# Kernel tuning notes

Measured on AMD Instinct MI355X. Metric: run time of the kernel, lower is better.

The kernel has to match this reference:

```python
import jax, jax.numpy as jnp
import numpy as np

EMBED, HIDDEN, VOCAB = 512, 512, 30000
B, S, K, NT = 16, 128, 49, 5


def _lin(x, W, b):
    # torch nn.Linear: y = x @ W.T + b, W stored as (out, in)
    return x @ W.T + b


def setup_inputs() -> dict:
    key = jax.random.key(0)
    ks = jax.random.split(key, 32)
    g = lambda i, shape, scale=0.05: (jax.random.normal(ks[i], shape, dtype=jnp.float32) * scale)
    inp = {
        "epoch": 30,
        "h_t": jax.random.normal(ks[0], (B, S, HIDDEN), dtype=jnp.float32),
        "V": jax.random.normal(ks[1], (B, K, HIDDEN), dtype=jnp.float32),
        "T": jax.random.normal(ks[2], (B, NT, EMBED), dtype=jnp.float32),
        "W_ZV": g(3, (49, HIDDEN)), "b_ZV": jnp.zeros((49,), jnp.float32),
        "W_Zh": g(4, (49, HIDDEN)), "b_Zh": jnp.zeros((49,), jnp.float32),
        "W_az": g(5, (1, 49)), "b_az": jnp.zeros((1,), jnp.float32),
        "W_QT": g(6, (5, EMBED)), "b_QT": jnp.zeros((5,), jnp.float32),
        "W_Qh": g(7, (5, HIDDEN)), "b_Qh": jnp.zeros((5,), jnp.float32),
        "W_bq": g(8, (1, 5)), "b_bq": jnp.zeros((1,), jnp.float32),
        "W_sq": g(9, (EMBED, EMBED)), "b_sq": jnp.zeros((EMBED,), jnp.float32),
        "W_sh": g(10, (EMBED, HIDDEN)), "b_sh": jnp.zeros((EMBED,), jnp.float32),
        "W_Ss": g(11, (5, EMBED)), "b_Ss": jnp.zeros((5,), jnp.float32),
        "W_Sr": g(12, (5, EMBED)), "b_Sr": jnp.zeros((5,), jnp.float32),
        "W_sz": g(13, (EMBED, HIDDEN)), "b_sz": jnp.zeros((EMBED,), jnp.float32),
        "W_mlp": g(14, (VOCAB, EMBED)), "b_mlp": jnp.zeros((VOCAB,), jnp.float32),
    }
    return inp


def reference(epoch, h_t, V, T,
              W_ZV, b_ZV, W_Zh, b_Zh, W_az, b_az,
              W_QT, b_QT, W_Qh, b_Qh, W_bq, b_bq,
              W_sq, b_sq, W_sh, b_sh, W_Ss, b_Ss,
              W_Sr, b_Sr, W_sz, b_sz, W_mlp, b_mlp):
    # --- visual attention (dropout = identity, eval mode) ---
    # content_V: [B, S, K, 49]
    content_V = _lin(V, W_ZV, b_ZV)[:, None, :, :] + _lin(h_t, W_Zh, b_Zh)[:, :, None, :]
    visual_t = (jnp.tanh(content_V) @ W_az.T + b_az)[..., 0]          # [B, S, K]
    alpha_t = jax.nn.softmax(visual_t, axis=-1)
    z_t = jnp.einsum('bsk,bkh->bsh', alpha_t, V)                      # [B, S, H]
    r_t = jnp.tanh(_lin(z_t, W_sz, b_sz))                             # [B, S, E]
    # --- topic attention ---
    content_T = _lin(T, W_QT, b_QT)[:, None, :, :] + _lin(h_t, W_Qh, b_Qh)[:, :, None, :]  # [B,S,5,5]
    topic_t = (jnp.tanh(content_T) @ W_bq.T + b_bq)[..., 0]           # [B, S, 5]
    beta_t = jax.nn.softmax(topic_t, axis=-1)
    q_t = jnp.einsum('bst,bte->bse', beta_t, T)                       # [B, S, E]
    s_t = jnp.tanh(_lin(q_t, W_sq, b_sq) + _lin(h_t, W_sh, b_sh))     # [B, S, E]
    # --- sentinel scores: the torch loop reduces to (batch 0, diagonal pos) only ---
    qh0 = _lin(h_t[0], W_Qh, b_Qh)                                    # [S, 5]
    score_s = jnp.tanh(_lin(s_t[0], W_Ss, b_Ss) + qh0) @ W_bq.T + b_bq  # [S, 1]
    score_r = jnp.tanh(_lin(r_t[0], W_Sr, b_Sr) + qh0) @ W_bq.T + b_bq  # [S, 1]
    if epoch <= 20:
        gama_t = 1.0
    else:
        gama_t = jax.nn.sigmoid(score_s - score_r)[None, :, :]        # [1, S, 1]
    c_t = gama_t * s_t + (1.0 - gama_t) * r_t                         # [B, S, E]
    scores = _lin(c_t, W_mlp, b_mlp)                                  # [B, S, vocab]
    return scores
```

## Files before the change

kernel.cpp:

```cpp
#include <hip/hip_runtime.h>
#include <hip/hip_bf16.h>


typedef short bf16x8 __attribute__((ext_vector_type(8)));
typedef float f32x4 __attribute__((ext_vector_type(4)));
typedef short short8 __attribute__((ext_vector_type(8)));

static __device__ __forceinline__ short f2bf(float f) {
    union { float f; unsigned u; } v; v.f = f;
    unsigned r = v.u + 0x7FFFu + ((v.u >> 16) & 1u);
    return (short)(r >> 16);
}

#define GLD_LDS16(gp, lp)                                                          \
    __builtin_amdgcn_global_load_lds(                                              \
        (const __attribute__((address_space(1))) unsigned int*)(gp),               \
        (__attribute__((address_space(3))) unsigned int*)(lp), 16, 0, 0)

__global__ __launch_bounds__(256) void k_front(
    const float* __restrict__ h, const float* __restrict__ V, const float* __restrict__ T,
    const float* __restrict__ W_Zh, const float* __restrict__ b_Zh,
    const float* __restrict__ W_Qh, const float* __restrict__ b_Qh,
    const float* __restrict__ W_ZV, const float* __restrict__ b_ZV,
    const float* __restrict__ W_QT, const float* __restrict__ b_QT,
    float* __restrict__ Zh, float* __restrict__ Qh,
    float* __restrict__ ZV, float* __restrict__ QT,
    const float* __restrict__ wmlp, short* __restrict__ wmlp_b,
    short* __restrict__ h_b,
    const float* __restrict__ wsz, short* __restrict__ wsz_b,
    const float* __restrict__ wsq, short* __restrict__ wsq_b,
    const float* __restrict__ wsh, short* __restrict__ wsh_b)
{
    __shared__ float xs[512];
    const int bid = blockIdx.x;
    const int t = threadIdx.x;

    if (bid < 2048) {
        const float* hp = h + (size_t)bid * 512;
        for (int i = t; i < 512; i += 256) xs[i] = hp[i];
        __syncthreads();
        if (t < 49) {
            const float* w = W_Zh + t * 512;
            float acc = b_Zh[t];
            #pragma unroll 8
            for (int i = 0; i < 512; ++i) acc = fmaf(xs[i], w[i], acc);
            Zh[bid * 64 + t] = acc;
        } else if (t >= 64 && t < 69) {
            const int o = t - 64;
            const float* w = W_Qh + o * 512;
            float acc = b_Qh[o];
            #pragma unroll 8
            for (int i = 0; i < 512; ++i) acc = fmaf(xs[i], w[i], acc);
            Qh[bid * 8 + o] = acc;
        }
        return;
    }
    if (bid < 2912) {
        const int blk = bid - 2048;
        if (blk < 784) {
            const float* xp = V + (size_t)blk * 512;
            for (int i = t; i < 512; i += 256) xs[i] = xp[i];
            __syncthreads();
            if (t < 49) {
                const float* w = W_ZV + t * 512;
                float acc = b_ZV[t];
                #pragma unroll 8
                for (int i = 0; i < 512; ++i) acc = fmaf(xs[i], w[i], acc);
                ZV[blk * 64 + t] = acc;
            }
        } else {
            const int row = blk - 784;
            const float* xp = T + (size_t)row * 512;
            for (int i = t; i < 512; i += 256) xs[i] = xp[i];
            __syncthreads();
            if (t < 5) {
                const float* w = W_QT + t * 512;
                float acc = b_QT[t];
                #pragma unroll 8
                for (int i = 0; i < 512; ++i) acc = fmaf(xs[i], w[i], acc);
                QT[row * 8 + t] = acc;
            }
        }
        return;
    }
    const float* src; short* dst; int i;
    if (bid < 10412)      { src = wmlp; dst = wmlp_b; i = (bid - 2912) * 256 + t; }
    else if (bid < 10924) { src = h;    dst = h_b;    i = (bid - 10412) * 256 + t; }
    else if (bid < 11052) { src = wsz;  dst = wsz_b;  i = (bid - 10924) * 256 + t; }
    else if (bid < 11180) { src = wsq;  dst = wsq_b;  i = (bid - 11052) * 256 + t; }
    else                  { src = wsh;  dst = wsh_b;  i = (bid - 11180) * 256 + t; }
    const float4 a = ((const float4*)src)[i * 2];
    const float4 b = ((const float4*)src)[i * 2 + 1];
    short8 o;
    o[0] = f2bf(a.x); o[1] = f2bf(a.y); o[2] = f2bf(a.z); o[3] = f2bf(a.w);
    o[4] = f2bf(b.x); o[5] = f2bf(b.y); o[6] = f2bf(b.z); o[7] = f2bf(b.w);
    ((short8*)dst)[i] = o;
}

__global__ void k_attn(const float* __restrict__ V, const float* __restrict__ T,
                       const float* __restrict__ ZV, const float* __restrict__ Zh,
                       const float* __restrict__ QT, const float* __restrict__ Qh,
                       const float* __restrict__ W_az, const float* __restrict__ b_az,
                       const float* __restrict__ W_bq, const float* __restrict__ b_bq,
                       short* __restrict__ z_bf, short* __restrict__ q_bf)
{
    const int row = blockIdx.x;
    const int b = row >> 7;
    const int t = threadIdx.x;
    __shared__ float zh[49], waz[49], alpha[49], beta[5];
    if (t < 49) { zh[t] = Zh[row * 64 + t]; waz[t] = W_az[t]; }
    __syncthreads();
    if (t < 49) {
        const float* zv = ZV + (b * 49 + t) * 64;
        float acc = b_az[0];
        for (int j = 0; j < 49; ++j) acc += tanhf(zv[j] + zh[j]) * waz[j];
        alpha[t] = acc;
    } else if (t >= 64 && t < 69) {
        const int tt = t - 64;
        const float* qt = QT + (b * 5 + tt) * 8;
        const float* qh = Qh + row * 8;
        float acc = b_bq[0];
        for (int j = 0; j < 5; ++j) acc += tanhf(qt[j] + qh[j]) * W_bq[j];
        beta[tt] = acc;
    }
    __syncthreads();
    const int wv = t >> 6, l = t & 63;
    if (wv == 0) {
        float a = (l < 49) ? alpha[l] : -1e30f;
        float m = a;
        #pragma unroll
        for (int off = 32; off; off >>= 1) m = fmaxf(m, __shfl_xor(m, off));
        float e = (l < 49) ? expf(a - m) : 0.f;
        float s = e;
        #pragma unroll
        for (int off = 32; off; off >>= 1) s += __shfl_xor(s, off);
        if (l < 49) alpha[l] = e / s;
    } else if (wv == 1) {
        float a = (l < 5) ? beta[l] : -1e30f;
        float m = a;
        #pragma unroll
        for (int off = 32; off; off >>= 1) m = fmaxf(m, __shfl_xor(m, off));
        float e = (l < 5) ? expf(a - m) : 0.f;
        float s = e;
        #pragma unroll
        for (int off = 32; off; off >>= 1) s += __shfl_xor(s, off);
        if (l < 5) beta[l] = e / s;
    }
    __syncthreads();
    const float* Vb = V + (size_t)b * 49 * 512;
    const float* Tb = T + (size_t)b * 5 * 512;
    for (int hd = t; hd < 512; hd += 256) {
        float az = 0.f;
        #pragma unroll
        for (int k = 0; k < 49; ++k) az = fmaf(alpha[k], Vb[k * 512 + hd], az);
        z_bf[(size_t)row * 512 + hd] = f2bf(az);
        float aq = 0.f;
        #pragma unroll
        for (int k = 0; k < 5; ++k) aq = fmaf(beta[k], Tb[k * 512 + hd], aq);
        q_bf[(size_t)row * 512 + hd] = f2bf(aq);
    }
}

__global__ __launch_bounds__(256) void k_rs(
    const short* __restrict__ Zb, const short* __restrict__ Qb, const short* __restrict__ Hb,
    const short* __restrict__ Wsz, const short* __restrict__ Wsq, const short* __restrict__ Wsh,
    const float* __restrict__ b_sz, const float* __restrict__ b_sq, const float* __restrict__ b_sh,
    float* __restrict__ r_t, float* __restrict__ s_t)
{
    constexpr int K = 512, NN = 512;
    __shared__ __align__(16) short sA[64 * 64];
    __shared__ __align__(16) short sW[64 * 64];
    const int tid = threadIdx.x;
    const int l = tid & 63, w = tid >> 6;
    const int m0 = blockIdx.x * 64, n0 = blockIdx.y * 64;
    const int wm = (w & 1) * 32, wn = (w >> 1) * 32;
    const int lm = l & 15, lg = l >> 4;
    const int sr = l >> 3, sc = l & 7;
    f32x4 accr[2][2] = {}, accs[2][2] = {};

#define RS_PASS(AG, WG, ACC)                                                      \
    for (int k0 = 0; k0 < K; k0 += 64) {                                          \
        _Pragma("unroll")                                                         \
        for (int c = 0; c < 2; ++c) {                                             \
            const int R = w * 16 + c * 8;                                         \
            const int row = R + sr;                                               \
            GLD_LDS16((AG) + (size_t)(m0 + row) * K + k0 + ((sc ^ (row & 7)) << 3), sA + R * 64); \
            GLD_LDS16((WG) + (size_t)(n0 + row) * K + k0 + ((sc ^ (row & 7)) << 3), sW + R * 64); \
        }                                                                         \
        __syncthreads();                                                          \
        bf16x8 af[2][2], bv[2][2];                                                \
        _Pragma("unroll")                                                         \
        for (int s = 0; s < 2; ++s)                                               \
            _Pragma("unroll")                                                     \
            for (int i = 0; i < 2; ++i) {                                         \
                const int ra = wm + i * 16 + lm;                                  \
                const int rb = wn + i * 16 + lm;                                  \
                af[s][i] = *(const bf16x8*)(sA + ra * 64 + (((s * 4 + lg) ^ (ra & 7)) << 3)); \
                bv[s][i] = *(const bf16x8*)(sW + rb * 64 + (((s * 4 + lg) ^ (rb & 7)) << 3)); \
            }                                                                     \
        _Pragma("unroll")                                                         \
        for (int s = 0; s < 2; ++s)                                               \
            _Pragma("unroll")                                                     \
            for (int i = 0; i < 2; ++i)                                           \
                _Pragma("unroll")                                                 \
                for (int j = 0; j < 2; ++j)                                       \
                    ACC[i][j] = __builtin_amdgcn_mfma_f32_16x16x32_bf16(af[s][i], bv[s][j], ACC[i][j], 0, 0, 0); \
        __syncthreads();                                                          \
    }

    RS_PASS(Zb, Wsz, accr)
    RS_PASS(Qb, Wsq, accs)
    RS_PASS(Hb, Wsh, accs)
#undef RS_PASS

    #pragma unroll
    for (int j = 0; j < 2; ++j) {
        const int n = n0 + wn + j * 16 + lm;
        const float br = b_sz[n];
        const float bs = b_sq[n] + b_sh[n];
        #pragma unroll
        for (int i = 0; i < 2; ++i) {
            const int m = m0 + wm + i * 16 + lg * 4;
            #pragma unroll
            for (int q = 0; q < 4; ++q) {
                r_t[(size_t)(m + q) * NN + n] = tanhf(accr[i][j][q] + br);
                s_t[(size_t)(m + q) * NN + n] = tanhf(accs[i][j][q] + bs);
            }
        }
    }
}

__global__ __launch_bounds__(256, 4) void k_gemm_mlp(
    const short* __restrict__ A, const short* __restrict__ Wb,
    const float* __restrict__ bias, float* __restrict__ C)
{
    constexpr int N = 30000, K = 512;
    __shared__ __align__(16) short shA[128 * 64];
    __shared__ __align__(16) short shW[128 * 64];
    const int tid = threadIdx.x;
    const int l = tid & 63, w = tid >> 6;
    const int bid = blockIdx.x;
    const int swz = (bid & 7) * 470 + (bid >> 3);
    const int m0 = (swz & 15) * 128;
    const int n0 = (swz >> 4) * 128;
    const int wm = (w & 1) * 64, wn = (w >> 1) * 64;
    const int lm = l & 15, lg = l >> 4;
    const int sr = tid >> 3, sc = tid & 7;
    const short* Ag = A  + (size_t)m0 * K;
    const short* Wg = Wb + (size_t)n0 * K;
    f32x4 acc[4][4] = {};

    for (int t = 0; t < 8; ++t) {
        const int kk = t * 64;
        #pragma unroll
        for (int c = 0; c < 4; ++c) {
            const int row = c * 32 + sr;
            GLD_LDS16(Ag + (size_t)row * K + kk + ((sc ^ (row & 7)) << 3),
                      &shA[(c * 32 + w * 8) * 64]);
            GLD_LDS16(Wg + (size_t)row * K + kk + ((sc ^ (row & 7)) << 3),
                      &shW[(c * 32 + w * 8) * 64]);
        }
        __syncthreads();
        bf16x8 af[2][4], bv[2][4];
        #pragma unroll
        for (int s = 0; s < 2; ++s)
            #pragma unroll
            for (int i = 0; i < 4; ++i) {
                const int ra = wm + i * 16 + lm;
                const int rb = wn + i * 16 + lm;
                const int ck = s * 4 + lg;
                af[s][i] = *(const bf16x8*)(&shA[ra * 64 + ((ck ^ (ra & 7)) << 3)]);
                bv[s][i] = *(const bf16x8*)(&shW[rb * 64 + ((ck ^ (rb & 7)) << 3)]);
            }
        #pragma unroll
        for (int s = 0; s < 2; ++s)
            #pragma unroll
            for (int i = 0; i < 4; ++i)
                #pragma unroll
                for (int j = 0; j < 4; ++j)
                    acc[i][j] = __builtin_amdgcn_mfma_f32_16x16x32_bf16(
                        af[s][i], bv[s][j], acc[i][j], 0, 0, 0);
        __syncthreads();
    }

    #pragma unroll
    for (int j = 0; j < 4; ++j) {
        const int n = n0 + wn + j * 16 + lm;
        if (n >= N) continue;
        const float bj = bias[n];
        #pragma unroll
        for (int i = 0; i < 4; ++i) {
            const int m = m0 + wm + i * 16 + lg * 4;
            #pragma unroll
            for (int q = 0; q < 4; ++q)
                __builtin_nontemporal_store(acc[i][j][q] + bj, &C[(size_t)(m + q) * N + n]);
        }
    }
}

__global__ __launch_bounds__(256) void k_blend_gate(
    const float* __restrict__ s_t, const float* __restrict__ r_t,
    const float* __restrict__ Qh,
    const float* __restrict__ W_Ss, const float* __restrict__ b_Ss,
    const float* __restrict__ W_Sr, const float* __restrict__ b_Sr,
    const float* __restrict__ W_bq, const float* __restrict__ b_bq,
    const int* __restrict__ epoch, short* __restrict__ c_bf)
{
    const int row = blockIdx.x;
    const int s = row & 127;
    const int t = threadIdx.x;
    float g = 1.0f;
    if (epoch[0] > 20) {
        const int l = t & 63;
        const int d = l * 8;
        const float4 s0 = *(const float4*)(s_t + (size_t)s * 512 + d);
        const float4 s1 = *(const float4*)(s_t + (size_t)s * 512 + d + 4);
        const float4 r0 = *(const float4*)(r_t + (size_t)s * 512 + d);
        const float4 r1 = *(const float4*)(r_t + (size_t)s * 512 + d + 4);
        float ss = b_bq[0], sr = b_bq[0];
        #pragma unroll
        for (int k = 0; k < 5; ++k) {
            const float4 w0 = *(const float4*)(W_Ss + k * 512 + d);
            const float4 w1 = *(const float4*)(W_Ss + k * 512 + d + 4);
            const float4 v0 = *(const float4*)(W_Sr + k * 512 + d);
            const float4 v1 = *(const float4*)(W_Sr + k * 512 + d + 4);
            float as = s0.x*w0.x + s0.y*w0.y + s0.z*w0.z + s0.w*w0.w
                     + s1.x*w1.x + s1.y*w1.y + s1.z*w1.z + s1.w*w1.w;
            float ar = r0.x*v0.x + r0.y*v0.y + r0.z*v0.z + r0.w*v0.w
                     + r1.x*v1.x + r1.y*v1.y + r1.z*v1.z + r1.w*v1.w;
            #pragma unroll
            for (int off = 32; off; off >>= 1) {
                as += __shfl_xor(as, off);
                ar += __shfl_xor(ar, off);
            }
            const float qh = Qh[s * 8 + k];
            ss += tanhf(as + b_Ss[k] + qh) * W_bq[k];
            sr += tanhf(ar + b_Sr[k] + qh) * W_bq[k];
        }
        g = 1.f / (1.f + expf(-(ss - sr)));
    }
    const size_t base = (size_t)row * 512;
    for (int i = t; i < 512; i += 256)
        c_bf[base + i] = f2bf(g * s_t[base + i] + (1.f - g) * r_t[base + i]);
}

extern "C" void kernel_launch(void* const* d_in, const int* in_sizes, int n_in,
                              void* d_out, int out_size, void* d_ws, size_t ws_size,
                              hipStream_t stream)
{
    const int*   epoch = (const int*)  d_in[0];
    const float* h_t   = (const float*)d_in[1];
    const float* V     = (const float*)d_in[2];
    const float* T     = (const float*)d_in[3];
    const float* W_ZV  = (const float*)d_in[4];  const float* b_ZV = (const float*)d_in[5];
    const float* W_Zh  = (const float*)d_in[6];  const float* b_Zh = (const float*)d_in[7];
    const float* W_az  = (const float*)d_in[8];  const float* b_az = (const float*)d_in[9];
    const float* W_QT  = (const float*)d_in[10]; const float* b_QT = (const float*)d_in[11];
    const float* W_Qh  = (const float*)d_in[12]; const float* b_Qh = (const float*)d_in[13];
    const float* W_bq  = (const float*)d_in[14]; const float* b_bq = (const float*)d_in[15];
    const float* W_sq  = (const float*)d_in[16]; const float* b_sq = (const float*)d_in[17];
    const float* W_sh  = (const float*)d_in[18]; const float* b_sh = (const float*)d_in[19];
    const float* W_Ss  = (const float*)d_in[20]; const float* b_Ss = (const float*)d_in[21];
    const float* W_Sr  = (const float*)d_in[22]; const float* b_Sr = (const float*)d_in[23];
    const float* W_sz  = (const float*)d_in[24]; const float* b_sz = (const float*)d_in[25];
    const float* W_mlp = (const float*)d_in[26]; const float* b_mlp= (const float*)d_in[27];

    float* out = (float*)d_out;
    float* ws  = (float*)d_ws;
    const size_t M1 = 1024 * 1024;
    float* r_t  = ws;
    float* s_t  = ws + M1;
    float* Zh   = ws + 2 * M1;
    float* ZV   = Zh + 2048 * 64;
    float* Qh   = ZV + 784 * 64;
    float* QT   = Qh + 2048 * 8;
    float* pad  = QT + 80 * 8;
    short* sreg = (short*)(pad + 128);
    short* z_bf   = sreg;
    short* q_bf   = z_bf + M1;
    short* h_bf   = q_bf + M1;
    short* c_bf   = h_bf + M1;
    short* Wsz_bf = c_bf + M1;
    short* Wsq_bf = Wsz_bf + 512 * 512;
    short* Wsh_bf = Wsq_bf + 512 * 512;
    short* W_bf   = Wsh_bf + 512 * 512;

    k_front<<<11308, 256, 0, stream>>>(h_t, V, T,
                                       W_Zh, b_Zh, W_Qh, b_Qh, W_ZV, b_ZV, W_QT, b_QT,
                                       Zh, Qh, ZV, QT,
                                       W_mlp, W_bf, h_bf,
                                       W_sz, Wsz_bf, W_sq, Wsq_bf, W_sh, Wsh_bf);
    k_attn<<<2048, 256, 0, stream>>>(V, T, ZV, Zh, QT, Qh, W_az, b_az, W_bq, b_bq, z_bf, q_bf);
    k_rs<<<dim3(32, 8), 256, 0, stream>>>(z_bf, q_bf, h_bf, Wsz_bf, Wsq_bf, Wsh_bf,
                                          b_sz, b_sq, b_sh, r_t, s_t);
    k_blend_gate<<<2048, 256, 0, stream>>>(s_t, r_t, Qh, W_Ss, b_Ss, W_Sr, b_Sr,
                                           W_bq, b_bq, epoch, c_bf);
    k_gemm_mlp<<<3760, 256, 0, stream>>>(c_bf, W_bf, b_mlp, out);
}
```

Measured before the change: 197.9 us.

## Move small attention projections to bf16 MFMA and enlarge MLP GEMM tiles

The scalar per-row FMA loops that computed Zh/Qh/ZV/QT in k_front are replaced by bf16 conversion of h, V, T and zero-padded packed weight blocks, followed by a new small MFMA GEMM kernel (k_linhv). Separately, the vocab GEMM is retiled from 128x128 with 256 threads to 256x256 with 512 threads, with 8x4 accumulator fragments per wave, to raise data reuse. This adds a kernel launch and lowers the front projections to bf16 precision. It also raises register and LDS pressure in the main GEMM, and with 944 blocks the last N tile wastes more work on padding.

```diff
diff --git a/kernel.cpp b/kernel.cpp
--- a/kernel.cpp
+++ b/kernel.cpp
@@ -19,82 +19,127 @@
 
 __global__ __launch_bounds__(256) void k_front(
     const float* __restrict__ h, const float* __restrict__ V, const float* __restrict__ T,
-    const float* __restrict__ W_Zh, const float* __restrict__ b_Zh,
-    const float* __restrict__ W_Qh, const float* __restrict__ b_Qh,
-    const float* __restrict__ W_ZV, const float* __restrict__ b_ZV,
-    const float* __restrict__ W_QT, const float* __restrict__ b_QT,
-    float* __restrict__ Zh, float* __restrict__ Qh,
-    float* __restrict__ ZV, float* __restrict__ QT,
-    const float* __restrict__ wmlp, short* __restrict__ wmlp_b,
-    short* __restrict__ h_b,
+    const float* __restrict__ W_Zh, const float* __restrict__ W_Qh,
+    const float* __restrict__ W_ZV, const float* __restrict__ W_QT,
+    short* __restrict__ P1, short* __restrict__ P2, short* __restrict__ P3,
+    short* __restrict__ V_b, short* __restrict__ T_b, short* __restrict__ h_b,
     const float* __restrict__ wsz, short* __restrict__ wsz_b,
     const float* __restrict__ wsq, short* __restrict__ wsq_b,
-    const float* __restrict__ wsh, short* __restrict__ wsh_b)
-{
-    __shared__ float xs[512];
+    const float* __restrict__ wsh, short* __restrict__ wsh_b,
+    const float* __restrict__ wmlp, short* __restrict__ wmlp_b)
+{
     const int bid = blockIdx.x;
     const int t = threadIdx.x;
 
-    if (bid < 2048) {
-        const float* hp = h + (size_t)bid * 512;
-        for (int i = t; i < 512; i += 256) xs[i] = hp[i];
-        __syncthreads();
-        if (t < 49) {
-            const float* w = W_Zh + t * 512;
-            float acc = b_Zh[t];
-            #pragma unroll 8
-            for (int i = 0; i < 512; ++i) acc = fmaf(xs[i], w[i], acc);
-            Zh[bid * 64 + t] = acc;
-        } else if (t >= 64 && t < 69) {
-            const int o = t - 64;
-            const float* w = W_Qh + o * 512;
-            float acc = b_Qh[o];
-            #pragma unroll 8
-            for (int i = 0; i < 512; ++i) acc = fmaf(xs[i], w[i], acc);
-            Qh[bid * 8 + o] = acc;
-        }
+    if (bid < 48) {
+        const int pid = bid >> 4, blk = bid & 15;
+        short* dst = (pid == 0) ? P1 : (pid == 1) ? P2 : P3;
+        const int base = blk * 2048 + t * 8;
+        const int r = base >> 9, c = base & 511;
+        const float* srow = nullptr;
+        if (pid == 0)      srow = (r < 49) ? (W_Zh + r * 512) : ((r < 54) ? (W_Qh + (r - 49) * 512) : nullptr);
+        else if (pid == 1) srow = (r < 49) ? (W_ZV + r * 512) : nullptr;
+        else               srow = (r < 5)  ? (W_QT + r * 512) : nullptr;
+        short8 o = {0, 0, 0, 0, 0, 0, 0, 0};
+        if (srow) {
+            const float4 a = *(const float4*)(srow + c);
+            const float4 b = *(const float4*)(srow + c + 4);
+            o[0] = f2bf(a.x); o[1] = f2bf(a.y); o[2] = f2bf(a.z); o[3] = f2bf(a.w);
+            o[4] = f2bf(b.x); o[5] = f2bf(b.y); o[6] = f2bf(b.z); o[7] = f2bf(b.w);
+        }
+        *(short8*)(dst + base) = o;
         return;
     }
-    if (bid < 2912) {
-        const int blk = bid - 2048;
-        if (blk < 784) {
-            const float* xp = V + (size_t)blk * 512;
-            for (int i = t; i < 512; i += 256) xs[i] = xp[i];
-            __syncthreads();
-            if (t < 49) {
-                const float* w = W_ZV + t * 512;
-                float acc = b_ZV[t];
-                #pragma unroll 8
-                for (int i = 0; i < 512; ++i) acc = fmaf(xs[i], w[i], acc);
-                ZV[blk * 64 + t] = acc;
-            }
-        } else {
-            const int row = blk - 784;
-            const float* xp = T + (size_t)row * 512;
-            for (int i = t; i < 512; i += 256) xs[i] = xp[i];
-            __syncthreads();
-            if (t < 5) {
-                const float* w = W_QT + t * 512;
-                float acc = b_QT[t];
-                #pragma unroll 8
-                for (int i = 0; i < 512; ++i) acc = fmaf(xs[i], w[i], acc);
-                QT[row * 8 + t] = acc;
-            }
-        }
-        return;
-    }
     const float* src; short* dst; int i;
-    if (bid < 10412)      { src = wmlp; dst = wmlp_b; i = (bid - 2912) * 256 + t; }
-    else if (bid < 10924) { src = h;    dst = h_b;    i = (bid - 10412) * 256 + t; }
-    else if (bid < 11052) { src = wsz;  dst = wsz_b;  i = (bid - 10924) * 256 + t; }
-    else if (bid < 11180) { src = wsq;  dst = wsq_b;  i = (bid - 11052) * 256 + t; }
-    else                  { src = wsh;  dst = wsh_b;  i = (bid - 11180) * 256 + t; }
+    if (bid < 244)       { src = V;    dst = V_b;    i = (bid - 48) * 256 + t; }
+    else if (bid < 264)  { src = T;    dst = T_b;    i = (bid - 244) * 256 + t; }
+    else if (bid < 776)  { src = h;    dst = h_b;    i = (bid - 264) * 256 + t; }
+    else if (bid < 904)  { src = wsz;  dst = wsz_b;  i = (bid - 776) * 256 + t; }
+    else if (bid < 1032) { src = wsq;  dst = wsq_b;  i = (bid - 904) * 256 + t; }
+    else if (bid < 1160) { src = wsh;  dst = wsh_b;  i = (bid - 1032) * 256 + t; }
+    else                 { src = wmlp; dst = wmlp_b; i = (bid - 1160) * 256 + t; }
     const float4 a = ((const float4*)src)[i * 2];
     const float4 b = ((const float4*)src)[i * 2 + 1];
     short8 o;
     o[0] = f2bf(a.x); o[1] = f2bf(a.y); o[2] = f2bf(a.z); o[3] = f2bf(a.w);
     o[4] = f2bf(b.x); o[5] = f2bf(b.y); o[6] = f2bf(b.z); o[7] = f2bf(b.w);
     ((short8*)dst)[i] = o;
+}
+
+__global__ __launch_bounds__(256) void k_linhv(
+    const short* __restrict__ h_b, const short* __restrict__ V_b, const short* __restrict__ T_b,
+    const short* __restrict__ P1, const short* __restrict__ P2, const short* __restrict__ P3,
+    const float* __restrict__ b_Zh, const float* __restrict__ b_Qh,
+    const float* __restrict__ b_ZV, const float* __restrict__ b_QT,
+    float* __restrict__ Zh, float* __restrict__ Qh,
+    float* __restrict__ ZV, float* __restrict__ QT)
+{
+    constexpr int K = 512;
+    const int bid = blockIdx.x;
+    int sect, m0;
+    const short *Ag, *Wg;
+    if (bid < 32)      { sect = 0; m0 = bid * 64;        Ag = h_b; Wg = P1; }
+    else if (bid < 45) { sect = 1; m0 = (bid - 32) * 64; Ag = V_b; Wg = P2; }
+    else               { sect = 2; m0 = (bid - 45) * 64; Ag = T_b; Wg = P3; }
+
+    __shared__ __align__(16) short sA[64 * 64];
+    __shared__ __align__(16) short sW[64 * 64];
+    const int tid = threadIdx.x;
+    const int l = tid & 63, w = tid >> 6;
+    const int wm = (w & 1) * 32, wn = (w >> 1) * 32;
+    const int lm = l & 15, lg = l >> 4;
+    const int sr = l >> 3, sc = l & 7;
+    f32x4 acc[2][2] = {};
+
+    for (int k0 = 0; k0 < K; k0 += 64) {
+        #pragma unroll
+        for (int c = 0; c < 2; ++c) {
+            const int R = w * 16 + c * 8;
+            const int row = R + sr;
+            GLD_LDS16(Ag + (size_t)(m0 + row) * K + k0 + ((sc ^ (row & 7)) << 3), sA + R * 64);
+            GLD_LDS16(Wg + (size_t)row * K + k0 + ((sc ^ (row & 7)) << 3), sW + R * 64);
+        }
+        __syncthreads();
+        bf16x8 af[2][2], bv[2][2];
+        #pragma unroll
+        for (int s = 0; s < 2; ++s)
+            #pragma unroll
+            for (int i = 0; i < 2; ++i) {
+                const int ra = wm + i * 16 + lm;
+                const int rb = wn + i * 16 + lm;
+                af[s][i] = *(const bf16x8*)(sA + ra * 64 + (((s * 4 + lg) ^ (ra & 7)) << 3));
+                bv[s][i] = *(const bf16x8*)(sW + rb * 64 + (((s * 4 + lg) ^ (rb & 7)) << 3));
+            }
+        #pragma unroll
+        for (int s = 0; s < 2; ++s)
+            #pragma unroll
+            for (int i = 0; i < 2; ++i)
+                #pragma unroll
+                for (int j = 0; j < 2; ++j)
+                    acc[i][j] = __builtin_amdgcn_mfma_f32_16x16x32_bf16(af[s][i], bv[s][j], acc[i][j], 0, 0, 0);
+        __syncthreads();
+    }
+
+    #pragma unroll
+    for (int j = 0; j < 2; ++j) {
+        const int n = wn + j * 16 + lm;
+        #pragma unroll
+        for (int i = 0; i < 2; ++i) {
+            #pragma unroll
+            for (int q = 0; q < 4; ++q) {
+                const int m = m0 + wm + i * 16 + lg * 4 + q;
+                const float v = acc[i][j][q];
+                if (sect == 0) {
+                    if (n < 49)      Zh[(size_t)m * 64 + n] = v + b_Zh[n];
+                    else if (n < 54) Qh[(size_t)m * 8 + (n - 49)] = v + b_Qh[n - 49];
+                } else if (sect == 1) {
+                    if (m < 784 && n < 49) ZV[(size_t)m * 64 + n] = v + b_ZV[n];
+                } else {
+                    if (m < 80 && n < 5) QT[(size_t)m * 8 + n] = v + b_QT[n];
+                }
+            }
+        }
+    }
 }
 
 __global__ void k_attn(const float* __restrict__ V, const float* __restrict__ T,
@@ -230,52 +275,55 @@
     }
 }
 
-__global__ __launch_bounds__(256, 4) void k_gemm_mlp(
+__global__ __launch_bounds__(512, 4) void k_gemm_mlp(
     const short* __restrict__ A, const short* __restrict__ Wb,
     const float* __restrict__ bias, float* __restrict__ C)
 {
     constexpr int N = 30000, K = 512;
-    __shared__ __align__(16) short shA[128 * 64];
-    __shared__ __align__(16) short shW[128 * 64];
+    __shared__ __align__(16) short shA[256 * 64];
+    __shared__ __align__(16) short shW[256 * 64];
     const int tid = threadIdx.x;
     const int l = tid & 63, w = tid >> 6;
     const int bid = blockIdx.x;
-    const int swz = (bid & 7) * 470 + (bid >> 3);
-    const int m0 = (swz & 15) * 128;
-    const int n0 = (swz >> 4) * 128;
-    const int wm = (w & 1) * 64, wn = (w >> 1) * 64;
+    const int swz = (bid & 7) * 118 + (bid >> 3);
+    const int m0 = (swz & 7) * 256;
+    const int n0 = (swz >> 3) * 256;
+    const int wm = (w >> 2) * 128, wn = (w & 3) * 64;
     const int lm = l & 15, lg = l >> 4;
-    const int sr = tid >> 3, sc = tid & 7;
+    const int lr = l >> 3, sc = l & 7;
     const short* Ag = A  + (size_t)m0 * K;
     const short* Wg = Wb + (size_t)n0 * K;
-    f32x4 acc[4][4] = {};
+    f32x4 acc[8][4] = {};
 
     for (int t = 0; t < 8; ++t) {
         const int kk = t * 64;
         #pragma unroll
         for (int c = 0; c < 4; ++c) {
-            const int row = c * 32 + sr;
+            const int row = c * 64 + w * 8 + lr;
             GLD_LDS16(Ag + (size_t)row * K + kk + ((sc ^ (row & 7)) << 3),
-                      &shA[(c * 32 + w * 8) * 64]);
+                      &shA[(c * 64 + w * 8) * 64]);
             GLD_LDS16(Wg + (size_t)row * K + kk + ((sc ^ (row & 7)) << 3),
-                      &shW[(c * 32 + w * 8) * 64]);
+                      &shW[(c * 64 + w * 8) * 64]);
         }
         __syncthreads();
-        bf16x8 af[2][4], bv[2][4];
+        bf16x8 af[2][8], bv[2][4];
+        #pragma unroll
+        for (int s = 0; s < 2; ++s) {
+            #pragma unroll
+            for (int i = 0; i < 8; ++i) {
+                const int ra = wm + i * 16 + lm;
+                af[s][i] = *(const bf16x8*)(&shA[ra * 64 + (((s * 4 + lg) ^ (ra & 7)) << 3)]);
+            }
+            #pragma unroll
+            for (int j = 0; j < 4; ++j) {
+                const int rb = wn + j * 16 + lm;
+                bv[s][j] = *(const bf16x8*)(&shW[rb * 64 + (((s * 4 + lg) ^ (rb & 7)) << 3)]);
+            }
+        }
         #pragma unroll
         for (int s = 0; s < 2; ++s)
             #pragma unroll
-            for (int i = 0; i < 4; ++i) {
-                const int ra = wm + i * 16 + lm;
-                const int rb = wn + i * 16 + lm;
-                const int ck = s * 4 + lg;
-                af[s][i] = *(const bf16x8*)(&shA[ra * 64 + ((ck ^ (ra & 7)) << 3)]);
-                bv[s][i] = *(const bf16x8*)(&shW[rb * 64 + ((ck ^ (rb & 7)) << 3)]);
-            }
-        #pragma unroll
-        for (int s = 0; s < 2; ++s)
-            #pragma unroll
-            for (int i = 0; i < 4; ++i)
+            for (int i = 0; i < 8; ++i)
                 #pragma unroll
                 for (int j = 0; j < 4; ++j)
                     acc[i][j] = __builtin_amdgcn_mfma_f32_16x16x32_bf16(
@@ -289,7 +337,7 @@
         if (n >= N) continue;
         const float bj = bias[n];
         #pragma unroll
-        for (int i = 0; i < 4; ++i) {
+        for (int i = 0; i < 8; ++i) {
             const int m = m0 + wm + i * 16 + lg * 4;
             #pragma unroll
             for (int q = 0; q < 4; ++q)
@@ -383,17 +431,23 @@
     short* Wsz_bf = c_bf + M1;
     short* Wsq_bf = Wsz_bf + 512 * 512;
     short* Wsh_bf = Wsq_bf + 512 * 512;
-    short* W_bf   = Wsh_bf + 512 * 512;
-
-    k_front<<<11308, 256, 0, stream>>>(h_t, V, T,
-                                       W_Zh, b_Zh, W_Qh, b_Qh, W_ZV, b_ZV, W_QT, b_QT,
-                                       Zh, Qh, ZV, QT,
-                                       W_mlp, W_bf, h_bf,
-                                       W_sz, Wsz_bf, W_sq, Wsq_bf, W_sh, Wsh_bf);
+    short* V_bf   = Wsh_bf + 512 * 512;
+    short* T_bf   = V_bf + 832 * 512;
+    short* P1     = T_bf + 128 * 512;
+    short* P2     = P1 + 64 * 512;
+    short* P3     = P2 + 64 * 512;
+    short* W_bf   = P3 + 64 * 512;
+
+    k_front<<<8660, 256, 0, stream>>>(h_t, V, T, W_Zh, W_Qh, W_ZV, W_QT,
+                                      P1, P2, P3, V_bf, T_bf, h_bf,
+                                      W_sz, Wsz_bf, W_sq, Wsq_bf, W_sh, Wsh_bf,
+                                      W_mlp, W_bf);
+    k_linhv<<<47, 256, 0, stream>>>(h_bf, V_bf, T_bf, P1, P2, P3,
+                                    b_Zh, b_Qh, b_ZV, b_QT, Zh, Qh, ZV, QT);
     k_attn<<<2048, 256, 0, stream>>>(V, T, ZV, Zh, QT, Qh, W_az, b_az, W_bq, b_bq, z_bf, q_bf);
     k_rs<<<dim3(32, 8), 256, 0, stream>>>(z_bf, q_bf, h_bf, Wsz_bf, Wsq_bf, Wsh_bf,
                                           b_sz, b_sq, b_sh, r_t, s_t);
     k_blend_gate<<<2048, 256, 0, stream>>>(s_t, r_t, Qh, W_Ss, b_Ss, W_Sr, b_Sr,
                                            W_bq, b_bq, epoch, c_bf);
-    k_gemm_mlp<<<3760, 256, 0, stream>>>(c_bf, W_bf, b_mlp, out);
-}
+    k_gemm_mlp<<<944, 512, 0, stream>>>(c_bf, W_bf, b_mlp, out);
+}
```

New measurement: 549.1 us. 2.78x slower.
